# Performance work log

Measured on AMD Instinct MI355X. Metric: run time of the kernel, lower is better.

Reference implementation:

```python
import jax, jax.numpy as jnp
import numpy as np

N_QUBITS = 14
N_LAYERS = 2
BATCH = 512


def _apply_ry(state, theta, wire):
    # state: [B, 2,...,2] (n_qubits axes of size 2); theta: [B] per-sample angle
    c = jnp.cos(theta * 0.5)[:, None]
    s = jnp.sin(theta * 0.5)[:, None]
    st = jnp.moveaxis(state, wire + 1, 1)
    shp = st.shape
    st = st.reshape(shp[0], 2, -1)
    a0, a1 = st[:, 0], st[:, 1]
    # RY = [[cos, -sin], [sin, cos]] (real matrix, so the state stays real)
    st = jnp.stack([c * a0 - s * a1, s * a0 + c * a1], axis=1)
    return jnp.moveaxis(st.reshape(shp), 1, wire + 1)


def _apply_cnot(state, ctrl, tgt):
    ca, ta = ctrl + 1, tgt + 1
    s0 = jnp.take(state, 0, axis=ca)
    s1 = jnp.take(state, 1, axis=ca)
    # flip target axis on the control=1 slice (axis index shifts if it was after ctrl)
    s1 = jnp.flip(s1, axis=ta if ta < ca else ta - 1)
    return jnp.stack([s0, s1], axis=ca)


def _circuit(x, weights):
    B, n = x.shape
    L = weights.shape[0]
    # |0...0> initial state, batched
    state = jnp.zeros((B,) + (2,) * n, x.dtype).at[(slice(None),) + (0,) * n].set(1.0)
    # angle encoding: RY(x[b, w]) on wire w
    for w in range(n):
        state = _apply_ry(state, x[:, w], w)
    # BasicEntanglerLayers: per layer, RY(weights[l, w]) on each wire, then CNOT ring
    for l in range(L):
        for w in range(n):
            state = _apply_ry(state, jnp.broadcast_to(weights[l, w], (B,)), w)
        for w in range(n):
            state = _apply_cnot(state, w, (w + 1) % n)
    # <Z_w> = P(bit_w = 0) - P(bit_w = 1)
    probs = state * state
    exps = []
    for w in range(n):
        p = jnp.moveaxis(probs, w + 1, 1).reshape(B, 2, -1).sum(-1)
        exps.append(p[:, 0] - p[:, 1])
    return jnp.stack(exps, axis=1)  # [B, n_qubits]


def setup_inputs() -> dict:
    key = jax.random.key(0)
    k1, k2 = jax.random.split(key)
    x = jax.random.normal(k1, (BATCH, N_QUBITS), dtype=jnp.float32)
    weights = (2.0 * np.pi) * jax.random.uniform(k2, (N_LAYERS, N_QUBITS), dtype=jnp.float32)
    return {"x": x, "weights": weights}


def reference(x, weights):
    return _circuit(x, weights)
```

## Files before the change

kernel.cpp:

```cpp
#include <hip/hip_runtime.h>

#define NQ 14
#define BLOCK 512
#define NG 28
#define NF2 16

typedef float f32x2 __attribute__((ext_vector_type(2)));
__device__ __forceinline__ f32x2 mk2(float a, float b) { f32x2 r; r.x = a; r.y = b; return r; }

struct Sched { unsigned m[NG]; unsigned r[NG]; unsigned fr[NQ]; };

constexpr Sched build_sched() {
  Sched sc{};
  unsigned col[NQ] = {}, rowinv[NQ] = {};
  for (int p = 0; p < NQ; ++p) { col[p] = 1u << p; rowinv[p] = 1u << p; }
  int g = 0;
  for (int l = 0; l < 2; ++l) {
    for (int w = 0; w < NQ; ++w) { int p = NQ - 1 - w; sc.m[g] = col[p]; sc.r[g] = rowinv[p]; ++g; }
    for (int w = 0; w < NQ; ++w) {
      int tgt = (w + 1) % NQ; int pc = NQ - 1 - w, pt = NQ - 1 - tgt;
      col[pc] ^= col[pt]; rowinv[pt] ^= rowinv[pc];
    }
  }
  for (int w = 0; w < NQ; ++w) sc.fr[w] = rowinv[NQ - 1 - w];
  return sc;
}
constexpr Sched SC = build_sched();

constexpr unsigned SPAN[4] = {0x3E00u, 0x03E0u, 0x003Eu, 0x3007u};

constexpr unsigned lmap1(unsigned v) { return ((v >> 9) & 1u) | (((v >> 10) & 15u) << 1); }
constexpr unsigned lmap2(unsigned v) { return ((v >> 9) & 1u) | (((v >> 5) & 15u) << 1); }
constexpr unsigned lmap3(unsigned v) { return ((v >> 5) & 1u) | (((v >> 1) & 15u) << 1); }
constexpr unsigned lmap4(unsigned v) {
  return ((v >> 1) & 1u) | (((v >> 2) & 1u) << 1) | ((v & 1u) << 2) | (((v >> 12) & 3u) << 3);
}

__host__ __device__ constexpr unsigned i1(unsigned t, unsigned p, unsigned e) { return t | (e << 9) | (p << 10); }
__host__ __device__ constexpr unsigned i2(unsigned t, unsigned p, unsigned e) {
  return (t & 31u) | (p << 5) | (e << 9) | ((t >> 5) << 10);
}
__host__ __device__ constexpr unsigned i3(unsigned t, unsigned p, unsigned e) {
  return (t & 1u) | (p << 1) | (e << 5) | ((t >> 1) << 6);
}
__host__ __device__ constexpr unsigned i4(unsigned t, unsigned p, unsigned e) {
  return ((p >> 1) & 1u) | (e << 1) | ((p & 1u) << 2) | (t << 3) | (((p >> 2) & 3u) << 12);
}
__host__ __device__ constexpr unsigned base1(unsigned t) { return t; }
__host__ __device__ constexpr unsigned base2(unsigned t) { return (t & 31u) | ((t >> 5) << 10); }
__host__ __device__ constexpr unsigned base3(unsigned t) { return (t & 1u) | ((t >> 1) << 6); }
__host__ __device__ constexpr unsigned base4(unsigned t) { return t << 3; }

__host__ __device__ constexpr unsigned a1(unsigned i) {
  const unsigned tA = i & 511u, jA = (i >> 11) & 7u;
  return 4u * (tA * 8u + (jA ^ (tA & 7u))) + ((i >> 9) & 1u) + 2u * ((i >> 10) & 1u);
}
__host__ __device__ constexpr unsigned a2(unsigned i) {
  const unsigned tB = (i & 31u) | (((i >> 10) & 15u) << 5);
  const unsigned jB = (i >> 6) & 7u;
  return 4u * (tB * 8u + (jB ^ (tB & 7u))) + ((i >> 5) & 1u) + 2u * ((i >> 9) & 1u);
}
__host__ __device__ constexpr unsigned a3(unsigned i) {
  const unsigned tC = (i >> 3) & 511u;
  const unsigned kC = (i & 1u) | (((i >> 12) & 3u) << 1);
  return 4u * (tC * 8u + (kC ^ ((i >> 6) & 7u))) + ((i >> 1) & 1u) + 2u * ((i >> 2) & 1u);
}

constexpr bool sched_ok() {
  for (int g = 0; g < 14; ++g)
    if (SC.m[g] != (1u << (13 - g)) || SC.r[g] != (1u << (13 - g))) return false;
  for (int g = 14; g < 28; ++g) {
    const int ph = (g < 18) ? 0 : (g < 22) ? 1 : (g < 26) ? 2 : 3;
    if (SC.m[g] & ~SPAN[ph]) return false;
    unsigned lm = 0, lr = 0;
    if (ph == 0) { lm = lmap1(SC.m[g]); lr = lmap1(SC.r[g]); }
    if (ph == 1) { lm = lmap2(SC.m[g]); lr = lmap2(SC.r[g]); }
    if (ph == 2) { lm = lmap3(SC.m[g]); lr = lmap3(SC.r[g]); }
    if (ph == 3) { lm = lmap4(SC.m[g]); lr = lmap4(SC.r[g]); }
    if (lm == 0) return false;
    if (!(__builtin_popcount(lm & lr) & 1)) return false;
  }
  return true;
}
static_assert(sched_ok(), "schedule invalid");

constexpr unsigned iP(int ph, unsigned t, unsigned p, unsigned e) {
  return ph == 0 ? i1(t, p, e) : ph == 1 ? i2(t, p, e) : ph == 2 ? i3(t, p, e) : i4(t, p, e);
}
constexpr bool layouts_ok() {
  for (int ph = 0; ph < 4; ++ph) {
    unsigned acc = 0;
    for (int k = 0; k < 14; ++k) {
      unsigned t = 0, p = 0, e = 0;
      if (k < 9) t = 1u << k; else if (k < 13) p = 1u << (k - 9); else e = 1;
      const unsigned v = iP(ph, t, p, e);
      if (__builtin_popcount(v) != 1 || (acc & v)) return false;
      acc |= v;
    }
    if (acc != 0x3FFFu) return false;
  }
  for (unsigned t = 0; t < 512; ++t) {
    if (base1(t) != i1(t, 0, 0) || base2(t) != i2(t, 0, 0)) return false;
    if (base3(t) != i3(t, 0, 0) || base4(t) != i4(t, 0, 0)) return false;
  }
  return true;
}
static_assert(layouts_ok(), "phase layouts invalid");

constexpr bool stmap_bij(int which) {
  bool hit[16384] = {};
  for (unsigned i = 0; i < 16384; ++i) {
    const unsigned a = which == 0 ? a1(i) : which == 1 ? a2(i) : a3(i);
    if (a >= 16384u || hit[a]) return false;
    hit[a] = true;
  }
  return true;
}
static_assert(stmap_bij(0), "a1 not bijective");
static_assert(stmap_bij(1), "a2 not bijective");
static_assert(stmap_bij(2), "a3 not bijective");

constexpr bool contig_ok(unsigned t0, unsigned t1) {
  for (unsigned t = t0; t < t1; ++t) {
    for (unsigned j = 0; j < 8; ++j) {
      const unsigned b1 = a1(i1(t, 2 * j, 0));
      if (b1 % 4 != 0) return false;
      for (unsigned q = 0; q < 2; ++q) for (unsigned e = 0; e < 2; ++e)
        if (a1(i1(t, 2 * j + q, e)) != b1 + 2 * q + e) return false;
      const unsigned b2 = a2(i2(t, 2 * j, 0));
      if (b2 % 4 != 0) return false;
      for (unsigned q = 0; q < 2; ++q) for (unsigned e = 0; e < 2; ++e)
        if (a2(i2(t, 2 * j + q, e)) != b2 + q + 2 * e) return false;
      const unsigned b4 = a3(i4(t, 2 * j, 0));
      if (b4 % 4 != 0) return false;
      for (unsigned q = 0; q < 2; ++q) for (unsigned e = 0; e < 2; ++e)
        if (a3(i4(t, 2 * j + q, e)) != b4 + 2 * q + e) return false;
    }
    for (unsigned j = 0; j < 4; ++j) for (unsigned e = 0; e < 2; ++e) {
      const unsigned b3 = a3(i3(t, 4 * j, e));
      if (b3 % 4 != 0) return false;
      for (unsigned q = 0; q < 4; ++q)
        if (a3(i3(t, 4 * j + q, e)) != b3 + q) return false;
    }
    for (unsigned p = 0; p < 16; ++p) {
      const unsigned r1 = a1(i2(t, p, 0));
      if (r1 % 2 != 0 || a1(i2(t, p, 1)) != r1 + 1) return false;
      const unsigned r2 = a2(i3(t, p, 0));
      if (r2 % 2 != 0 || a2(i3(t, p, 1)) != r2 + 1) return false;
    }
  }
  return true;
}
static_assert(contig_ok(0, 64) && contig_ok(64, 128), "contig 0-128");
static_assert(contig_ok(128, 192) && contig_ok(192, 256), "contig 128-256");
static_assert(contig_ok(256, 320) && contig_ok(320, 384), "contig 256-384");
static_assert(contig_ok(384, 448) && contig_ok(448, 512), "contig 384-512");

constexpr bool banks128(int pat) {
  for (unsigned W = 0; W < 8; ++W)
    for (unsigned j = 0; j < 8; ++j) {
      int cnt[8] = {};
      for (unsigned l = 0; l < 64; ++l) {
        const unsigned t = W * 64u + l;
        unsigned a = 0;
        if (pat == 0) a = a1(i1(t, 2 * j, 0));
        if (pat == 1) a = a2(i2(t, 2 * j, 0));
        if (pat == 2) a = a3(i3(t, 4 * (j >> 1), j & 1));
        if (pat == 3) a = a3(i4(t, 2 * j, 0));
        if (++cnt[(a >> 2) & 7u] > 8) return false;
      }
    }
  return true;
}
constexpr bool banks64(int pat) {
  for (unsigned W = 0; W < 8; ++W)
    for (unsigned p = 0; p < 16; ++p) {
      int cnt[16] = {};
      for (unsigned l = 0; l < 64; ++l) {
        const unsigned t = W * 64u + l;
        const unsigned a = (pat == 0) ? a1(i2(t, p, 0)) : a2(i3(t, p, 0));
        if (++cnt[(a >> 1) & 15u] > 4) return false;
      }
    }
  return true;
}
static_assert(banks128(0), "T1w banks");
static_assert(banks128(1), "T2w banks");
static_assert(banks128(2), "T3w banks");
static_assert(banks128(3), "T3r banks");
static_assert(banks64(0), "T1r banks");
static_assert(banks64(1), "T2r banks");

template <unsigned MU, unsigned RHO>
__device__ __forceinline__ void gate_pk(f32x2* v, const float cg, const float sb) {
  const f32x2 C = mk2(cg, cg);
  constexpr unsigned M2 = MU >> 1;
  constexpr bool ODD = (MU & 1u) != 0;
  if constexpr (!ODD) {
    constexpr unsigned LSB = M2 & (0u - M2);
#pragma unroll
    for (unsigned p = 0; p < NF2; ++p) {
      if (p & LSB) continue;
      const unsigned q = p ^ M2;
      const int s0 = __builtin_popcount((2u * p) & RHO) & 1;
      const int s1 = __builtin_popcount((2u * p + 1u) & RHO) & 1;
      const f32x2 Sp = mk2(s0 ? -sb : sb, s1 ? -sb : sb);
      const f32x2 Xp = v[p], Xq = v[q];
      v[p] = C * Xp - Sp * Xq;
      v[q] = C * Xq + Sp * Xp;
    }
  } else if constexpr (M2 == 0) {
#pragma unroll
    for (unsigned p = 0; p < NF2; ++p) {
      const int s0 = __builtin_popcount((2u * p) & RHO) & 1;
      const f32x2 Sp = mk2(s0 ? -sb : sb, s0 ? sb : -sb);
      const f32x2 X = v[p];
      v[p] = C * X - Sp * mk2(X.y, X.x);
    }
  } else {
    constexpr unsigned LSB = M2 & (0u - M2);
#pragma unroll
    for (unsigned p = 0; p < NF2; ++p) {
      if (p & LSB) continue;
      const unsigned q = p ^ M2;
      const int s0 = __builtin_popcount((2u * p) & RHO) & 1;
      const int s1 = __builtin_popcount((2u * p + 1u) & RHO) & 1;
      const f32x2 Sp = mk2(s0 ? -sb : sb, s1 ? -sb : sb);
      const f32x2 Xp = v[p], Xq = v[q];
      const f32x2 T = Sp * Xp;
      v[p] = C * Xp - Sp * mk2(Xq.y, Xq.x);
      v[q] = C * Xq + mk2(T.y, T.x);
    }
  }
}

__global__ __launch_bounds__(BLOCK, 4) void qnn_kernel(
    const float* __restrict__ x, const float* __restrict__ wts,
    float* __restrict__ out) {
  __shared__ float4 S4[4096];
  float* const S = (float*)S4;
  float4* const F4 = S4;
  const f32x2* const Fv = (const f32x2*)S4;
  const unsigned t = threadIdx.x;
  const int b = blockIdx.x;

  f32x2 v2[NF2];

  {
    float cxx[NQ], sxx[NQ];
#pragma unroll
    for (int w = 0; w < NQ; ++w)
      __sincosf(0.5f * (x[b * NQ + w] + wts[w]), &sxx[w], &cxx[w]);
    float pl = 1.0f;
#pragma unroll
    for (int bb = 0; bb < 9; ++bb) pl *= ((t >> bb) & 1) ? sxx[13 - bb] : cxx[13 - bb];
    v2[0] = mk2(pl * cxx[4], pl * sxx[4]);
#pragma unroll
    for (int k = 0; k < 4; ++k) {
      const int K = 1 << k;
      const float sk = sxx[3 - k], ck = cxx[3 - k];
#pragma unroll
      for (int j = K - 1; j >= 0; --j) {
        v2[j | K] = v2[j] * mk2(sk, sk);
        v2[j] = v2[j] * mk2(ck, ck);
      }
    }
  }

#define RUN_GATE(LM, G, BASEPAR)                                          \
  {                                                                       \
    float sn, cs;                                                         \
    __sincosf(0.5f * wts[G], &sn, &cs);                                   \
    const float sb =                                                      \
        (__builtin_popcount((BASEPAR) & SC.r[G]) & 1) ? -sn : sn;         \
    gate_pk<LM(SC.m[G]), LM(SC.r[G])>(v2, cs, sb);                        \
  }

  {
    const unsigned bs = base1(t);
    RUN_GATE(lmap1, 14, bs) RUN_GATE(lmap1, 15, bs)
    RUN_GATE(lmap1, 16, bs) RUN_GATE(lmap1, 17, bs)
#pragma unroll
    for (unsigned j = 0; j < 8; ++j) {
      float4 w4;
      w4.x = v2[2 * j].x; w4.y = v2[2 * j].y;
      w4.z = v2[2 * j + 1].x; w4.w = v2[2 * j + 1].y;
      F4[a1(i1(t, 2 * j, 0)) >> 2] = w4;
    }
  }
  __syncthreads();

  {
    const unsigned bs = base2(t);
#pragma unroll
    for (unsigned p = 0; p < NF2; ++p) v2[p] = Fv[a1(i2(t, p, 0)) >> 1];
    RUN_GATE(lmap2, 18, bs) RUN_GATE(lmap2, 19, bs)
    RUN_GATE(lmap2, 20, bs) RUN_GATE(lmap2, 21, bs)
  }
  __syncthreads();
  {
#pragma unroll
    for (unsigned j = 0; j < 8; ++j) {
      float4 w4;
      w4.x = v2[2 * j].x; w4.y = v2[2 * j + 1].x;
      w4.z = v2[2 * j].y; w4.w = v2[2 * j + 1].y;
      F4[a2(i2(t, 2 * j, 0)) >> 2] = w4;
    }
  }
  __syncthreads();

  {
    const unsigned bs = base3(t);
#pragma unroll
    for (unsigned p = 0; p < NF2; ++p) v2[p] = Fv[a2(i3(t, p, 0)) >> 1];
    RUN_GATE(lmap3, 22, bs) RUN_GATE(lmap3, 23, bs)
    RUN_GATE(lmap3, 24, bs) RUN_GATE(lmap3, 25, bs)
  }
  __syncthreads();
  {
#pragma unroll
    for (unsigned j = 0; j < 4; ++j) {
      float4 w0, w1;
      w0.x = v2[4 * j].x; w0.y = v2[4 * j + 1].x; w0.z = v2[4 * j + 2].x; w0.w = v2[4 * j + 3].x;
      w1.x = v2[4 * j].y; w1.y = v2[4 * j + 1].y; w1.z = v2[4 * j + 2].y; w1.w = v2[4 * j + 3].y;
      F4[a3(i3(t, 4 * j, 0)) >> 2] = w0;
      F4[a3(i3(t, 4 * j, 1)) >> 2] = w1;
    }
  }
  __syncthreads();

  float ex[NQ];
  {
    const unsigned bs = base4(t);
#pragma unroll
    for (unsigned j = 0; j < 8; ++j) {
      const float4 r4 = F4[a3(i4(t, 2 * j, 0)) >> 2];
      v2[2 * j] = mk2(r4.x, r4.y);
      v2[2 * j + 1] = mk2(r4.z, r4.w);
    }
    RUN_GATE(lmap4, 26, bs) RUN_GATE(lmap4, 27, bs)

#pragma unroll
    for (unsigned p = 0; p < NF2; ++p) v2[p] = v2[p] * v2[p];
#pragma unroll
    for (int k = 0; k < 4; ++k) {
      const unsigned K = 1u << k;
#pragma unroll
      for (unsigned p = 0; p < NF2; ++p) {
        if (p & K) continue;
        const f32x2 A = v2[p], Bv = v2[p ^ K];
        v2[p] = A + Bv;
        v2[p ^ K] = A - Bv;
      }
    }
#pragma unroll
    for (int w = 0; w < NQ; ++w) {
      const unsigned ls = lmap4(SC.fr[w]);
      const f32x2 W = v2[ls >> 1];
      const float coef = (ls & 1u) ? (W.x - W.y) : (W.x + W.y);
      const int tf = __builtin_popcount(bs & SC.fr[w]) & 1;
      ex[w] = tf ? -coef : coef;
    }
  }

#pragma unroll
  for (int w = 0; w < NQ; ++w) {
#pragma unroll
    for (int off = 32; off > 0; off >>= 1) ex[w] += __shfl_xor(ex[w], off, 64);
  }
  __syncthreads();
  const unsigned lane = t & 63u, wv = t >> 6;
  if (lane == 0) {
#pragma unroll
    for (int w = 0; w < NQ; ++w) S[wv * NQ + w] = ex[w];
  }
  __syncthreads();
  if (t < NQ) {
    float r = 0.0f;
#pragma unroll
    for (int W = 0; W < 8; ++W) r += S[W * NQ + t];
    out[b * NQ + t] = r;
  }
#undef RUN_GATE
}

extern "C" void kernel_launch(void* const* d_in, const int* in_sizes, int n_in,
                              void* d_out, int out_size, void* d_ws, size_t ws_size,
                              hipStream_t stream) {
  const float* x = (const float*)d_in[0];
  const float* weights = (const float*)d_in[1];
  float* out = (float*)d_out;
  const int B = in_sizes[0] / NQ;
  qnn_kernel<<<B, BLOCK, 0, stream>>>(x, weights, out);
}
```

Before: 65.84 us.

## Redesign LDS transpose layouts and replace shuffle reduction with LDS tree

Replaces the shared-memory address maps for the three state transposes with new swizzled layouts. The per-thread base addresses are now computed once, and reads use simple OR/XOR offsets, which cuts address arithmetic and keeps LDS banks balanced, as checked by compile-time asserts. The final per-qubit expectation reduction now goes through shared memory in two staged passes instead of 14×6 wavefront shuffles. The sincos intrinsic is also split into separate sin/cos calls. The new reduction adds barriers and serial LDS sums, which could offset the savings from the cheaper addressing.

```diff
diff --git a/kernel.cpp b/kernel.cpp
--- a/kernel.cpp
+++ b/kernel.cpp
@@ -36,7 +36,9 @@
   return ((v >> 1) & 1u) | (((v >> 2) & 1u) << 1) | ((v & 1u) << 2) | (((v >> 12) & 3u) << 3);
 }
 
-__host__ __device__ constexpr unsigned i1(unsigned t, unsigned p, unsigned e) { return t | (e << 9) | (p << 10); }
+__host__ __device__ constexpr unsigned i1(unsigned t, unsigned p, unsigned e) {
+  return t | (e << 9) | (p << 10);
+}
 __host__ __device__ constexpr unsigned i2(unsigned t, unsigned p, unsigned e) {
   return (t & 31u) | (p << 5) | (e << 9) | ((t >> 5) << 10);
 }
@@ -51,19 +53,38 @@
 __host__ __device__ constexpr unsigned base3(unsigned t) { return (t & 1u) | ((t >> 1) << 6); }
 __host__ __device__ constexpr unsigned base4(unsigned t) { return t << 3; }
 
-__host__ __device__ constexpr unsigned a1(unsigned i) {
-  const unsigned tA = i & 511u, jA = (i >> 11) & 7u;
-  return 4u * (tA * 8u + (jA ^ (tA & 7u))) + ((i >> 9) & 1u) + 2u * ((i >> 10) & 1u);
-}
-__host__ __device__ constexpr unsigned a2(unsigned i) {
-  const unsigned tB = (i & 31u) | (((i >> 10) & 15u) << 5);
-  const unsigned jB = (i >> 6) & 7u;
-  return 4u * (tB * 8u + (jB ^ (tB & 7u))) + ((i >> 5) & 1u) + 2u * ((i >> 9) & 1u);
-}
-__host__ __device__ constexpr unsigned a3(unsigned i) {
-  const unsigned tC = (i >> 3) & 511u;
-  const unsigned kC = (i & 1u) | (((i >> 12) & 3u) << 1);
-  return 4u * (tC * 8u + (kC ^ ((i >> 6) & 7u))) + ((i >> 1) & 1u) + 2u * ((i >> 2) & 1u);
+__host__ __device__ constexpr unsigned dwT1(unsigned i) {
+  return ((i >> 9) & 1u) + 2u * ((i >> 10) & 1u)
+       + 4u * ((((i >> 11) & 7u) ^ (i & 7u)) | ((i & 511u) << 3));
+}
+__host__ __device__ constexpr unsigned dwT2(unsigned i) {
+  return ((i >> 5) & 1u) + 2u * ((i >> 6) & 1u)
+       + 4u * ((((i >> 7) & 7u) ^ (i & 7u)) | ((i & 31u) << 3) | (((i >> 10) & 15u) << 8));
+}
+__host__ __device__ constexpr unsigned dwT3(unsigned i) {
+  return ((i >> 1) & 1u) + 2u * ((i >> 2) & 1u)
+       + 4u * ((((i >> 3) & 7u) ^ ((i >> 6) & 7u)) | ((i & 1u) << 3) | (((i >> 6) & 255u) << 4));
+}
+
+__host__ __device__ constexpr unsigned W1(unsigned t, unsigned k) {
+  return (t << 3) | (k ^ (t & 7u));
+}
+__host__ __device__ constexpr unsigned BASER1(unsigned t) {
+  return ((t >> 5) & 1u) | (((((t >> 6) & 7u) ^ (t & 7u))) << 1) | ((t & 31u) << 4);
+}
+__host__ __device__ constexpr unsigned W2(unsigned t, unsigned j, unsigned e) {
+  return ((t & 7u) ^ (j | (e << 2))) | ((t & 31u) << 3) | (((t >> 5) & 15u) << 8);
+}
+__host__ __device__ constexpr unsigned CR2(unsigned t) {
+  return ((t >> 1) & 1u) | (((((t >> 2) & 7u) ^ (t & 1u))) << 1) | ((t & 1u) << 4)
+       | (((t >> 5) & 15u) << 9);
+}
+__host__ __device__ constexpr unsigned VR2(unsigned p) { return ((p & 3u) << 2) ^ (p << 5); }
+__host__ __device__ constexpr unsigned W3(unsigned t, unsigned j, unsigned e) {
+  return (((t >> 1) & 7u) ^ (j | (e << 2))) | ((t & 1u) << 3) | ((t >> 1) << 4);
+}
+__host__ __device__ constexpr unsigned R3(unsigned t, unsigned m) {
+  return (((t & 7u) ^ ((t >> 3) & 7u)) | ((t >> 3) << 4)) | (((m & 1u) << 3) | ((m >> 1) << 10));
 }
 
 constexpr bool sched_ok() {
@@ -77,7 +98,7 @@
     if (ph == 1) { lm = lmap2(SC.m[g]); lr = lmap2(SC.r[g]); }
     if (ph == 2) { lm = lmap3(SC.m[g]); lr = lmap3(SC.r[g]); }
     if (ph == 3) { lm = lmap4(SC.m[g]); lr = lmap4(SC.r[g]); }
-    if (lm == 0) return false;
+    if (lm == 0 || lm >= 32) return false;
     if (!(__builtin_popcount(lm & lr) & 1)) return false;
   }
   return true;
@@ -110,86 +131,99 @@
 constexpr bool stmap_bij(int which) {
   bool hit[16384] = {};
   for (unsigned i = 0; i < 16384; ++i) {
-    const unsigned a = which == 0 ? a1(i) : which == 1 ? a2(i) : a3(i);
+    const unsigned a = which == 0 ? dwT1(i) : which == 1 ? dwT2(i) : dwT3(i);
     if (a >= 16384u || hit[a]) return false;
     hit[a] = true;
   }
   return true;
 }
-static_assert(stmap_bij(0), "a1 not bijective");
-static_assert(stmap_bij(1), "a2 not bijective");
-static_assert(stmap_bij(2), "a3 not bijective");
-
-constexpr bool contig_ok(unsigned t0, unsigned t1) {
+static_assert(stmap_bij(0), "dwT1 not bijective");
+static_assert(stmap_bij(1), "dwT2 not bijective");
+static_assert(stmap_bij(2), "dwT3 not bijective");
+
+constexpr bool chk(int pat, unsigned t0, unsigned t1) {
   for (unsigned t = t0; t < t1; ++t) {
-    for (unsigned j = 0; j < 8; ++j) {
-      const unsigned b1 = a1(i1(t, 2 * j, 0));
-      if (b1 % 4 != 0) return false;
-      for (unsigned q = 0; q < 2; ++q) for (unsigned e = 0; e < 2; ++e)
-        if (a1(i1(t, 2 * j + q, e)) != b1 + 2 * q + e) return false;
-      const unsigned b2 = a2(i2(t, 2 * j, 0));
-      if (b2 % 4 != 0) return false;
-      for (unsigned q = 0; q < 2; ++q) for (unsigned e = 0; e < 2; ++e)
-        if (a2(i2(t, 2 * j + q, e)) != b2 + q + 2 * e) return false;
-      const unsigned b4 = a3(i4(t, 2 * j, 0));
-      if (b4 % 4 != 0) return false;
-      for (unsigned q = 0; q < 2; ++q) for (unsigned e = 0; e < 2; ++e)
-        if (a3(i4(t, 2 * j + q, e)) != b4 + 2 * q + e) return false;
-    }
-    for (unsigned j = 0; j < 4; ++j) for (unsigned e = 0; e < 2; ++e) {
-      const unsigned b3 = a3(i3(t, 4 * j, e));
-      if (b3 % 4 != 0) return false;
-      for (unsigned q = 0; q < 4; ++q)
-        if (a3(i3(t, 4 * j + q, e)) != b3 + q) return false;
-    }
-    for (unsigned p = 0; p < 16; ++p) {
-      const unsigned r1 = a1(i2(t, p, 0));
-      if (r1 % 2 != 0 || a1(i2(t, p, 1)) != r1 + 1) return false;
-      const unsigned r2 = a2(i3(t, p, 0));
-      if (r2 % 2 != 0 || a2(i3(t, p, 1)) != r2 + 1) return false;
+    if (pat == 0) {
+      for (unsigned k = 0; k < 8; ++k) {
+        const unsigned B = 4u * W1(t, k);
+        if (B + 3 >= 16384u) return false;
+        for (unsigned q = 0; q < 2; ++q)
+          for (unsigned e = 0; e < 2; ++e)
+            if (dwT1(i1(t, 2 * k + q, e)) != B + 2 * q + e) return false;
+      }
+    } else if (pat == 1) {
+      for (unsigned p = 0; p < 16; ++p) {
+        const unsigned s = BASER1(t) | (p << 9);
+        if (2 * s + 1 >= 16384u) return false;
+        for (unsigned e = 0; e < 2; ++e)
+          if (dwT1(i2(t, p, e)) != 2 * s + e) return false;
+      }
+    } else if (pat == 2) {
+      for (unsigned j = 0; j < 4; ++j)
+        for (unsigned e = 0; e < 2; ++e) {
+          const unsigned B = 4u * W2(t, j, e);
+          if (B + 3 >= 16384u) return false;
+          for (unsigned d = 0; d < 4; ++d)
+            if (dwT2(i2(t, 4 * j + d, e)) != B + d) return false;
+        }
+    } else if (pat == 3) {
+      for (unsigned p = 0; p < 16; ++p) {
+        const unsigned s = CR2(t) ^ VR2(p);
+        if (2 * s + 1 >= 16384u) return false;
+        for (unsigned e = 0; e < 2; ++e)
+          if (dwT2(i3(t, p, e)) != 2 * s + e) return false;
+      }
+    } else if (pat == 4) {
+      for (unsigned j = 0; j < 4; ++j)
+        for (unsigned e = 0; e < 2; ++e) {
+          const unsigned B = 4u * W3(t, j, e);
+          if (B + 3 >= 16384u) return false;
+          for (unsigned d = 0; d < 4; ++d)
+            if (dwT3(i3(t, 4 * j + d, e)) != B + d) return false;
+        }
+    } else {
+      for (unsigned m = 0; m < 8; ++m) {
+        const unsigned B = 4u * R3(t, m);
+        if (B + 3 >= 16384u) return false;
+        for (unsigned q = 0; q < 2; ++q)
+          for (unsigned e = 0; e < 2; ++e)
+            if (dwT3(i4(t, 2 * m + q, e)) != B + 2 * q + e) return false;
+      }
     }
   }
   return true;
 }
-static_assert(contig_ok(0, 64) && contig_ok(64, 128), "contig 0-128");
-static_assert(contig_ok(128, 192) && contig_ok(192, 256), "contig 128-256");
-static_assert(contig_ok(256, 320) && contig_ok(320, 384), "contig 256-384");
-static_assert(contig_ok(384, 448) && contig_ok(448, 512), "contig 384-512");
-
-constexpr bool banks128(int pat) {
-  for (unsigned W = 0; W < 8; ++W)
-    for (unsigned j = 0; j < 8; ++j) {
-      int cnt[8] = {};
+static_assert(chk(0, 0, 256) && chk(0, 256, 512), "T1w addr");
+static_assert(chk(1, 0, 256) && chk(1, 256, 512), "T1r addr");
+static_assert(chk(2, 0, 256) && chk(2, 256, 512), "T2w addr");
+static_assert(chk(3, 0, 256) && chk(3, 256, 512), "T2r addr");
+static_assert(chk(4, 0, 256) && chk(4, 256, 512), "T3w addr");
+static_assert(chk(5, 0, 256) && chk(5, 256, 512), "T3r addr");
+
+constexpr bool banks_ok() {
+  for (unsigned W = 0; W < 8; ++W) {
+    for (unsigned s = 0; s < 8; ++s) {
+      int c1[8] = {}, c2[8] = {}, c3[8] = {}, c4[8] = {};
       for (unsigned l = 0; l < 64; ++l) {
         const unsigned t = W * 64u + l;
-        unsigned a = 0;
-        if (pat == 0) a = a1(i1(t, 2 * j, 0));
-        if (pat == 1) a = a2(i2(t, 2 * j, 0));
-        if (pat == 2) a = a3(i3(t, 4 * (j >> 1), j & 1));
-        if (pat == 3) a = a3(i4(t, 2 * j, 0));
-        if (++cnt[(a >> 2) & 7u] > 8) return false;
-      }
-    }
-  return true;
-}
-constexpr bool banks64(int pat) {
-  for (unsigned W = 0; W < 8; ++W)
+        if (++c1[W1(t, s) & 7u] > 8) return false;
+        if (++c2[W2(t, s & 3u, s >> 2) & 7u] > 8) return false;
+        if (++c3[W3(t, s & 3u, s >> 2) & 7u] > 8) return false;
+        if (++c4[R3(t, s) & 7u] > 8) return false;
+      }
+    }
     for (unsigned p = 0; p < 16; ++p) {
-      int cnt[16] = {};
+      int c1[16] = {}, c2[16] = {};
       for (unsigned l = 0; l < 64; ++l) {
         const unsigned t = W * 64u + l;
-        const unsigned a = (pat == 0) ? a1(i2(t, p, 0)) : a2(i3(t, p, 0));
-        if (++cnt[(a >> 1) & 15u] > 4) return false;
-      }
-    }
+        if (++c1[(BASER1(t) | (p << 9)) & 15u] > 4) return false;
+        if (++c2[(CR2(t) ^ VR2(p)) & 15u] > 4) return false;
+      }
+    }
+  }
   return true;
 }
-static_assert(banks128(0), "T1w banks");
-static_assert(banks128(1), "T2w banks");
-static_assert(banks128(2), "T3w banks");
-static_assert(banks128(3), "T3r banks");
-static_assert(banks64(0), "T1r banks");
-static_assert(banks64(1), "T2r banks");
+static_assert(banks_ok(), "bank balance");
 
 template <unsigned MU, unsigned RHO>
 __device__ __forceinline__ void gate_pk(f32x2* v, const float cg, const float sb) {
@@ -240,7 +274,7 @@
   __shared__ float4 S4[4096];
   float* const S = (float*)S4;
   float4* const F4 = S4;
-  const f32x2* const Fv = (const f32x2*)S4;
+  f32x2* const Fv = (f32x2*)S4;
   const unsigned t = threadIdx.x;
   const int b = blockIdx.x;
 
@@ -249,8 +283,11 @@
   {
     float cxx[NQ], sxx[NQ];
 #pragma unroll
-    for (int w = 0; w < NQ; ++w)
-      __sincosf(0.5f * (x[b * NQ + w] + wts[w]), &sxx[w], &cxx[w]);
+    for (int w = 0; w < NQ; ++w) {
+      const float ang = 0.5f * (x[b * NQ + w] + wts[w]);
+      sxx[w] = __sinf(ang);
+      cxx[w] = __cosf(ang);
+    }
     float pl = 1.0f;
 #pragma unroll
     for (int bb = 0; bb < 9; ++bb) pl *= ((t >> bb) & 1) ? sxx[13 - bb] : cxx[13 - bb];
@@ -269,8 +306,8 @@
 
 #define RUN_GATE(LM, G, BASEPAR)                                          \
   {                                                                       \
-    float sn, cs;                                                         \
-    __sincosf(0.5f * wts[G], &sn, &cs);                                   \
+    const float ang = 0.5f * wts[G];                                      \
+    const float sn = __sinf(ang), cs = __cosf(ang);                       \
     const float sb =                                                      \
         (__builtin_popcount((BASEPAR) & SC.r[G]) & 1) ? -sn : sn;         \
     gate_pk<LM(SC.m[G]), LM(SC.r[G])>(v2, cs, sb);                        \
@@ -281,40 +318,22 @@
     RUN_GATE(lmap1, 14, bs) RUN_GATE(lmap1, 15, bs)
     RUN_GATE(lmap1, 16, bs) RUN_GATE(lmap1, 17, bs)
 #pragma unroll
-    for (unsigned j = 0; j < 8; ++j) {
+    for (unsigned k = 0; k < 8; ++k) {
       float4 w4;
-      w4.x = v2[2 * j].x; w4.y = v2[2 * j].y;
-      w4.z = v2[2 * j + 1].x; w4.w = v2[2 * j + 1].y;
-      F4[a1(i1(t, 2 * j, 0)) >> 2] = w4;
+      w4.x = v2[2 * k].x; w4.y = v2[2 * k].y;
+      w4.z = v2[2 * k + 1].x; w4.w = v2[2 * k + 1].y;
+      F4[W1(t, k)] = w4;
     }
   }
   __syncthreads();
 
   {
     const unsigned bs = base2(t);
-#pragma unroll
-    for (unsigned p = 0; p < NF2; ++p) v2[p] = Fv[a1(i2(t, p, 0)) >> 1];
+    const unsigned rb = BASER1(t);
+#pragma unroll
+    for (unsigned p = 0; p < NF2; ++p) v2[p] = Fv[rb | (p << 9)];
     RUN_GATE(lmap2, 18, bs) RUN_GATE(lmap2, 19, bs)
     RUN_GATE(lmap2, 20, bs) RUN_GATE(lmap2, 21, bs)
-  }
-  __syncthreads();
-  {
-#pragma unroll
-    for (unsigned j = 0; j < 8; ++j) {
-      float4 w4;
-      w4.x = v2[2 * j].x; w4.y = v2[2 * j + 1].x;
-      w4.z = v2[2 * j].y; w4.w = v2[2 * j + 1].y;
-      F4[a2(i2(t, 2 * j, 0)) >> 2] = w4;
-    }
-  }
-  __syncthreads();
-
-  {
-    const unsigned bs = base3(t);
-#pragma unroll
-    for (unsigned p = 0; p < NF2; ++p) v2[p] = Fv[a2(i3(t, p, 0)) >> 1];
-    RUN_GATE(lmap3, 22, bs) RUN_GATE(lmap3, 23, bs)
-    RUN_GATE(lmap3, 24, bs) RUN_GATE(lmap3, 25, bs)
   }
   __syncthreads();
   {
@@ -323,8 +342,29 @@
       float4 w0, w1;
       w0.x = v2[4 * j].x; w0.y = v2[4 * j + 1].x; w0.z = v2[4 * j + 2].x; w0.w = v2[4 * j + 3].x;
       w1.x = v2[4 * j].y; w1.y = v2[4 * j + 1].y; w1.z = v2[4 * j + 2].y; w1.w = v2[4 * j + 3].y;
-      F4[a3(i3(t, 4 * j, 0)) >> 2] = w0;
-      F4[a3(i3(t, 4 * j, 1)) >> 2] = w1;
+      F4[W2(t, j, 0)] = w0;
+      F4[W2(t, j, 1)] = w1;
+    }
+  }
+  __syncthreads();
+
+  {
+    const unsigned bs = base3(t);
+    const unsigned rb = CR2(t);
+#pragma unroll
+    for (unsigned p = 0; p < NF2; ++p) v2[p] = Fv[rb ^ VR2(p)];
+    RUN_GATE(lmap3, 22, bs) RUN_GATE(lmap3, 23, bs)
+    RUN_GATE(lmap3, 24, bs) RUN_GATE(lmap3, 25, bs)
+  }
+  __syncthreads();
+  {
+#pragma unroll
+    for (unsigned j = 0; j < 4; ++j) {
+      float4 w0, w1;
+      w0.x = v2[4 * j].x; w0.y = v2[4 * j + 1].x; w0.z = v2[4 * j + 2].x; w0.w = v2[4 * j + 3].x;
+      w1.x = v2[4 * j].y; w1.y = v2[4 * j + 1].y; w1.z = v2[4 * j + 2].y; w1.w = v2[4 * j + 3].y;
+      F4[W3(t, j, 0)] = w0;
+      F4[W3(t, j, 1)] = w1;
     }
   }
   __syncthreads();
@@ -333,10 +373,10 @@
   {
     const unsigned bs = base4(t);
 #pragma unroll
-    for (unsigned j = 0; j < 8; ++j) {
-      const float4 r4 = F4[a3(i4(t, 2 * j, 0)) >> 2];
-      v2[2 * j] = mk2(r4.x, r4.y);
-      v2[2 * j + 1] = mk2(r4.z, r4.w);
+    for (unsigned m = 0; m < 8; ++m) {
+      const float4 r4 = F4[R3(t, m)];
+      v2[2 * m] = mk2(r4.x, r4.y);
+      v2[2 * m + 1] = mk2(r4.z, r4.w);
     }
     RUN_GATE(lmap4, 26, bs) RUN_GATE(lmap4, 27, bs)
 
@@ -356,29 +396,38 @@
 #pragma unroll
     for (int w = 0; w < NQ; ++w) {
       const unsigned ls = lmap4(SC.fr[w]);
-      const f32x2 W = v2[ls >> 1];
-      const float coef = (ls & 1u) ? (W.x - W.y) : (W.x + W.y);
+      const f32x2 Wv = v2[ls >> 1];
+      const float coef = (ls & 1u) ? (Wv.x - Wv.y) : (Wv.x + Wv.y);
       const int tf = __builtin_popcount(bs & SC.fr[w]) & 1;
       ex[w] = tf ? -coef : coef;
     }
   }
-
-#pragma unroll
-  for (int w = 0; w < NQ; ++w) {
-#pragma unroll
-    for (int off = 32; off > 0; off >>= 1) ex[w] += __shfl_xor(ex[w], off, 64);
-  }
-  __syncthreads();
-  const unsigned lane = t & 63u, wv = t >> 6;
-  if (lane == 0) {
-#pragma unroll
-    for (int w = 0; w < NQ; ++w) S[wv * NQ + w] = ex[w];
+  __syncthreads();
+
+  {
+#pragma unroll
+    for (unsigned q = 0; q < 7; ++q)
+      Fv[t * 8u + (q ^ ((t >> 1) & 7u))] = mk2(ex[2 * q], ex[2 * q + 1]);
+  }
+  __syncthreads();
+  {
+    const unsigned w = t & 15u, g = t >> 4;
+    if (w < NQ) {
+      float acc = 0.0f;
+#pragma unroll
+      for (unsigned k = 0; k < 16; ++k)
+        acc += S[(g * 16u + k) * 16u + (((w & 14u) ^ (k & 14u)) + (w & 1u))];
+      S[8192u + w * 32u + g] = acc;
+    }
   }
   __syncthreads();
   if (t < NQ) {
     float r = 0.0f;
 #pragma unroll
-    for (int W = 0; W < 8; ++W) r += S[W * NQ + t];
+    for (unsigned j = 0; j < 8; ++j) {
+      const float4 r4 = F4[2048u + t * 8u + j];
+      r += r4.x + r4.y + r4.z + r4.w;
+    }
     out[b * NQ + t] = r;
   }
 #undef RUN_GATE
```

After: 63.49 us. 3.6% less time.
